# Kernel tuning notes

Hardware: AMD Instinct MI355X
Metric: run time of the kernel (lower is better)

The kernel has to match this reference:

```python
import jax, jax.numpy as jnp
import numpy as np

D_MODEL = 1024
NUM_HEADS = 16
D_K = D_MODEL // NUM_HEADS
THETA = 10000.0
BATCH = 4
SEQ = 2048


def _apply_rope(t, positions, theta):
    # t: (B, H, S, d_k); positions: (S,) int
    d_k = t.shape[-1]
    inv_freq = theta ** (-jnp.arange(0, d_k, 2, dtype=jnp.float32) / d_k)  # (d_k/2,)
    angles = positions.astype(jnp.float32)[:, None] * inv_freq[None, :]    # (S, d_k/2)
    cos = jnp.cos(angles)
    sin = jnp.sin(angles)
    x1 = t[..., 0::2]
    x2 = t[..., 1::2]
    r1 = x1 * cos - x2 * sin
    r2 = x1 * sin + x2 * cos
    # interleave back to (..., d_k)
    return jnp.stack([r1, r2], axis=-1).reshape(t.shape)


def setup_inputs() -> dict:
    key = jax.random.key(0)
    k0, k1, k2, k3, k4 = jax.random.split(key, 5)
    scale = 1.0 / np.sqrt(D_MODEL)
    return {
        "x": jax.random.normal(k0, (BATCH, SEQ, D_MODEL), dtype=jnp.float32),
        "wq": jax.random.normal(k1, (D_MODEL, D_MODEL), dtype=jnp.float32) * scale,
        "wk": jax.random.normal(k2, (D_MODEL, D_MODEL), dtype=jnp.float32) * scale,
        "wv": jax.random.normal(k3, (D_MODEL, D_MODEL), dtype=jnp.float32) * scale,
        "wo": jax.random.normal(k4, (D_MODEL, D_MODEL), dtype=jnp.float32) * scale,
        "token_positions": jnp.arange(SEQ, dtype=jnp.int32),
    }


def reference(x, wq, wk, wv, wo, token_positions):
    B, S, _ = x.shape
    H, dk = NUM_HEADS, D_K

    def proj(w):
        # Linear: y = x @ w.T, then split heads -> (B, H, S, d_k)
        y = jnp.einsum("bsd,ed->bse", x, w)
        return y.reshape(B, S, H, dk).transpose(0, 2, 1, 3)

    q = proj(wq)
    k = proj(wk)
    v = proj(wv)

    q = _apply_rope(q, token_positions, THETA)
    k = _apply_rope(k, token_positions, THETA)

    scores = jnp.einsum("bhqd,bhkd->bhqk", q, k) / jnp.sqrt(jnp.float32(dk))
    causal = jnp.tril(jnp.ones((S, S), dtype=bool))  # (S, S)
    scores = jnp.where(causal[None, None, :, :], scores, -jnp.inf)
    attn = jax.nn.softmax(scores, axis=-1)
    out = jnp.einsum("bhqk,bhkd->bhqd", attn, v)        # (B, H, S, d_k)
    out = out.transpose(0, 2, 1, 3).reshape(B, S, H * dk)
    return jnp.einsum("bse,de->bsd", out, wo)
```

## Files before the change

kernel.cpp:

```cpp
#include <hip/hip_runtime.h>
#include <hip/hip_bf16.h>

#define D_MODEL 1024
#define NHEADS 16
#define DKH 64
#define BATCH 4
#define SEQ 2048
#define BH_ (BATCH*NHEADS)
#define MROWS (BATCH*SEQ)

typedef __attribute__((ext_vector_type(8))) short bf16x8;
typedef __attribute__((ext_vector_type(4))) float f32x4;
typedef __attribute__((ext_vector_type(4))) short short4v;

static __device__ __forceinline__ unsigned short f2b(float f){
  union { float f; unsigned u; } v; v.f = f;
  unsigned u = v.u;
  return (unsigned short)((u + 0x7FFFu + ((u >> 16) & 1u)) >> 16);
}
static __device__ __forceinline__ float b2f(unsigned short h){
  union { unsigned u; float f; } v; v.u = ((unsigned)h) << 16; return v.f;
}

static __device__ __forceinline__ f32x4 mfma16(bf16x8 a, bf16x8 b, f32x4 c){
  return __builtin_amdgcn_mfma_f32_16x16x32_bf16(a, b, c, 0, 0, 0);
}

__global__ void cvt_bf16_kernel(const float* __restrict__ src,
                                unsigned short* __restrict__ dst, int n4){
  int i = blockIdx.x*blockDim.x + threadIdx.x;
  if (i >= n4) return;
  float4 f = ((const float4*)src)[i];
  short4v o;
  o.x = (short)f2b(f.x); o.y = (short)f2b(f.y);
  o.z = (short)f2b(f.z); o.w = (short)f2b(f.w);
  ((short4v*)dst)[i] = o;
}

#define BM 128
#define BN 128
#define BKG 64

template<int MODE>
__global__ __launch_bounds__(256) void gemm_nt(const unsigned short* __restrict__ A,
                                               const unsigned short* __restrict__ Bw,
                                               void* __restrict__ C,
                                               int M, int N, int K)
{
  __shared__ unsigned short As[BM*BKG];
  __shared__ unsigned short Bs[BN*BKG];
  const int t = threadIdx.x;
  const int lane = t & 63;
  const int wv = t >> 6;
  const int wr = wv >> 1, wc = wv & 1;
  const int l15 = lane & 15, l4 = lane >> 4;
  const int m0 = blockIdx.y*BM, n0 = blockIdx.x*BN;

  f32x4 acc[4][4] = {};

  int lrow[4], lsw[4], lke[4];
  #pragma unroll
  for (int i = 0; i < 4; ++i){
    int lin = t*64 + i*16;
    int row = lin >> 7;
    int koff = lin & 127;
    lrow[i] = row;
    lke[i]  = koff >> 1;
    lsw[i]  = row*128 + (koff ^ ((row & 7) << 4));
  }

  bf16x8 ra[4], rb[4];
  #pragma unroll
  for (int i = 0; i < 4; ++i){
    ra[i] = *(const bf16x8*)(A  + (size_t)(m0 + lrow[i])*K + lke[i]);
    rb[i] = *(const bf16x8*)(Bw + (size_t)(n0 + lrow[i])*K + lke[i]);
  }

  for (int kt = 0; kt < K; kt += BKG){
    if (kt) __syncthreads();
    #pragma unroll
    for (int i = 0; i < 4; ++i){
      *(bf16x8*)((char*)As + lsw[i]) = ra[i];
      *(bf16x8*)((char*)Bs + lsw[i]) = rb[i];
    }
    if (kt + BKG < K){
      #pragma unroll
      for (int i = 0; i < 4; ++i){
        ra[i] = *(const bf16x8*)(A  + (size_t)(m0 + lrow[i])*K + kt + BKG + lke[i]);
        rb[i] = *(const bf16x8*)(Bw + (size_t)(n0 + lrow[i])*K + kt + BKG + lke[i]);
      }
    }
    __syncthreads();
    #pragma unroll
    for (int kk = 0; kk < 2; ++kk){
      bf16x8 af[4], bfr[4];
      #pragma unroll
      for (int mi = 0; mi < 4; ++mi){
        int row = wr*64 + mi*16 + l15;
        int koff = kk*64 + l4*16;
        af[mi] = *(const bf16x8*)((const char*)As + row*128 + (koff ^ ((row & 7) << 4)));
      }
      #pragma unroll
      for (int ni = 0; ni < 4; ++ni){
        int row = wc*64 + ni*16 + l15;
        int koff = kk*64 + l4*16;
        bfr[ni] = *(const bf16x8*)((const char*)Bs + row*128 + (koff ^ ((row & 7) << 4)));
      }
      #pragma unroll
      for (int mi = 0; mi < 4; ++mi)
        #pragma unroll
        for (int ni = 0; ni < 4; ++ni)
          acc[mi][ni] = mfma16(af[mi], bfr[ni], acc[mi][ni]);
    }
  }

  #pragma unroll
  for (int mi = 0; mi < 4; ++mi)
    #pragma unroll
    for (int ni = 0; ni < 4; ++ni)
      #pragma unroll
      for (int r = 0; r < 4; ++r){
        int row = m0 + wr*64 + mi*16 + l4*4 + r;
        int col = n0 + wc*64 + ni*16 + l15;
        float v = acc[mi][ni][r];
        if (MODE == 0){
          int b = row >> 11, s = row & (SEQ-1);
          int h = col >> 6,  d = col & (DKH-1);
          ((unsigned short*)C)[((size_t)(b*NHEADS + h)*SEQ + s)*DKH + d] = f2b(v);
        } else {
          ((float*)C)[(size_t)row*N + col] = v;
        }
      }
}

__global__ void rope_kernel(unsigned int* __restrict__ qk,
                            const int* __restrict__ pos, int npairs){
  int i = blockIdx.x*blockDim.x + threadIdx.x;
  if (i >= npairs) return;
  int j = i & (DKH/2 - 1);
  int s = (i >> 5) & (SEQ-1);
  float p = (float)pos[s];
  float fr = expf(-((float)(2*j) * (1.0f/DKH)) * 9.210340371976184f);
  float ang = p * fr;
  float sn, cs;
  sincosf(ang, &sn, &cs);
  unsigned u = qk[i];
  float x1 = b2f((unsigned short)(u & 0xFFFFu));
  float x2 = b2f((unsigned short)(u >> 16));
  float r1 = x1*cs - x2*sn;
  float r2 = x1*sn + x2*cs;
  qk[i] = (unsigned)f2b(r1) | ((unsigned)f2b(r2) << 16);
}

__global__ void vtrans_kernel(const unsigned short* __restrict__ vin,
                              unsigned short* __restrict__ vt){
  __shared__ unsigned short tile[64][65];
  int bh = blockIdx.y;
  int s0 = blockIdx.x * 64;
  const unsigned short* src = vin + ((size_t)bh*SEQ + s0)*DKH;
  for (int i = threadIdx.x; i < 64*64; i += 256)
    tile[i >> 6][i & 63] = src[(size_t)(i >> 6)*DKH + (i & 63)];
  __syncthreads();
  unsigned short* dst = vt + (size_t)bh*DKH*SEQ + s0;
  for (int i = threadIdx.x; i < 64*64; i += 256)
    dst[(size_t)(i >> 6)*SEQ + (i & 63)] = tile[i & 63][i >> 6];
}

#define QW 32
#define QB 128
#define KVB 64

__global__ __launch_bounds__(256, 2) void attn_kernel(const unsigned short* __restrict__ Q,
                                                      const unsigned short* __restrict__ Kw,
                                                      const unsigned short* __restrict__ Vt,
                                                      unsigned short* __restrict__ Ob)
{
  __shared__ unsigned short Ks[2][KVB*64];
  __shared__ unsigned short Vs[2][KVB*64];
  __shared__ unsigned short Ps[4][QW*KVB];

  const int t = threadIdx.x;
  const int lane = t & 63;
  const int wv = t >> 6;
  const int l15 = lane & 15, l4 = lane >> 4;

  const int bid = blockIdx.x;
  const int bh = bid & (BH_-1);
  const int qt = (SEQ/QB - 1) - (bid >> 6);
  const int q0 = qt * QB;
  const int qw0 = q0 + wv*QW;

  const unsigned short* kg = Kw + (size_t)bh*SEQ*DKH;
  const unsigned short* vg = Vt + (size_t)bh*DKH*SEQ;
  const unsigned short* qg = Q  + ((size_t)bh*SEQ + qw0)*DKH;

  bf16x8 qa[2][2];
  #pragma unroll
  for (int qi = 0; qi < 2; ++qi)
    #pragma unroll
    for (int c = 0; c < 2; ++c)
      qa[qi][c] = *(const bf16x8*)(qg + (qi*16 + l15)*DKH + c*32 + l4*8);

  float m_r[2] = {-1e30f, -1e30f};
  float l_r[2] = {0.f, 0.f};
  f32x4 oacc[2][4] = {};

  const int srow = t >> 3;
  const int scb  = (t & 7) * 16;
  const int sko  = scb ^ ((srow & 7) << 4);
  const size_t vstride = (size_t)SEQ * 2;

  const int ntB   = q0/KVB + 2;
  const int twmax = (qw0 + QW - 1) >> 6;

  bf16x8 kl0, kl1, vl0, vl1;
  {
    const char* ksrc = (const char*)kg;
    const char* vsrc = (const char*)vg;
    kl0 = *(const bf16x8*)(ksrc + srow*128 + sko);
    kl1 = *(const bf16x8*)(ksrc + (srow+32)*128 + sko);
    vl0 = *(const bf16x8*)(vsrc + (size_t)srow*vstride + sko);
    vl1 = *(const bf16x8*)(vsrc + (size_t)(srow+32)*vstride + sko);
    *(bf16x8*)((char*)Ks[0] + srow*128 + scb)      = kl0;
    *(bf16x8*)((char*)Ks[0] + (srow+32)*128 + scb) = kl1;
    *(bf16x8*)((char*)Vs[0] + srow*128 + scb)      = vl0;
    *(bf16x8*)((char*)Vs[0] + (srow+32)*128 + scb) = vl1;
  }

  for (int tt = 0; tt < ntB; ++tt){
    const int cur = tt & 1;
    __syncthreads();
    const bool pre = (tt + 1 < ntB);
    if (pre){
      const size_t kvoff = (size_t)(tt+1) * KVB;
      const char* ksrc = (const char*)kg + kvoff*128;
      const char* vsrc = (const char*)vg + kvoff*2;
      kl0 = *(const bf16x8*)(ksrc + srow*128 + sko);
      kl1 = *(const bf16x8*)(ksrc + (srow+32)*128 + sko);
      vl0 = *(const bf16x8*)(vsrc + (size_t)srow*vstride + sko);
      vl1 = *(const bf16x8*)(vsrc + (size_t)(srow+32)*vstride + sko);
    }

    if (tt <= twmax){
      const char* kb = (const char*)Ks[cur];
      const char* vb = (const char*)Vs[cur];
      char* pb = (char*)Ps[wv];
      const int sw = (l15 & 7) << 4;

      f32x4 sacc[4][2];
      #pragma unroll
      for (int kt = 0; kt < 4; ++kt){
        const int krow = kt*16 + l15;
        bf16x8 kf0 = *(const bf16x8*)(kb + krow*128 + ((l4*16) ^ sw));
        bf16x8 kf1 = *(const bf16x8*)(kb + krow*128 + ((64 + l4*16) ^ sw));
        #pragma unroll
        for (int qi = 0; qi < 2; ++qi){
          f32x4 a = {};
          a = mfma16(kf0, qa[qi][0], a);
          a = mfma16(kf1, qa[qi][1], a);
          sacc[kt][qi] = a;
        }
      }

      const int kv0 = tt * KVB;
      #pragma unroll
      for (int qi = 0; qi < 2; ++qi){
        const int qrow = qw0 + qi*16 + l15;
        float p[16];
        float mloc = -1e30f;
        #pragma unroll
        for (int kt = 0; kt < 4; ++kt)
          #pragma unroll
          for (int r = 0; r < 4; ++r){
            int kvg = kv0 + kt*16 + l4*4 + r;
            float x = sacc[kt][qi][r] * 0.125f;
            x = (kvg > qrow) ? -1e30f : x;
            p[kt*4+r] = x;
            mloc = fmaxf(mloc, x);
          }
        mloc = fmaxf(mloc, __shfl_xor(mloc, 16));
        mloc = fmaxf(mloc, __shfl_xor(mloc, 32));
        float mn = fmaxf(m_r[qi], mloc);
        float alpha = __expf(m_r[qi] - mn);
        m_r[qi] = mn;
        float rs = 0.f;
        #pragma unroll
        for (int i = 0; i < 16; ++i){ p[i] = __expf(p[i] - mn); rs += p[i]; }
        rs += __shfl_xor(rs, 16);
        rs += __shfl_xor(rs, 32);
        l_r[qi] = l_r[qi]*alpha + rs;
        float ar[4];
        #pragma unroll
        for (int r = 0; r < 4; ++r) ar[r] = __shfl(alpha, l4*4 + r);
        #pragma unroll
        for (int dt = 0; dt < 4; ++dt)
          #pragma unroll
          for (int r = 0; r < 4; ++r) oacc[qi][dt][r] *= ar[r];
        char* pr = pb + (qi*16 + l15)*128;
        #pragma unroll
        for (int kt = 0; kt < 4; ++kt){
          unsigned u0, u1;
          asm("v_cvt_pk_bf16_f32 %0, %1, %2" : "=v"(u0) : "v"(p[kt*4+0]), "v"(p[kt*4+1]));
          asm("v_cvt_pk_bf16_f32 %0, %1, %2" : "=v"(u1) : "v"(p[kt*4+2]), "v"(p[kt*4+3]));
          unsigned long long uu = (unsigned long long)u0 | ((unsigned long long)u1 << 32);
          *(unsigned long long*)(pr + ((kt*32 + l4*8) ^ sw)) = uu;
        }
      }

      bf16x8 pa[2][2];
      #pragma unroll
      for (int qi = 0; qi < 2; ++qi){
        const char* pr = pb + (qi*16 + l15)*128;
        pa[qi][0] = *(const bf16x8*)(pr + ((l4*16) ^ sw));
        pa[qi][1] = *(const bf16x8*)(pr + ((64 + l4*16) ^ sw));
      }

      #pragma unroll
      for (int dt = 0; dt < 4; ++dt){
        const int vrow = dt*16 + l15;
        bf16x8 vf0 = *(const bf16x8*)(vb + vrow*128 + ((l4*16) ^ sw));
        bf16x8 vf1 = *(const bf16x8*)(vb + vrow*128 + ((64 + l4*16) ^ sw));
        #pragma unroll
        for (int qi = 0; qi < 2; ++qi){
          oacc[qi][dt] = mfma16(pa[qi][0], vf0, oacc[qi][dt]);
          oacc[qi][dt] = mfma16(pa[qi][1], vf1, oacc[qi][dt]);
        }
      }
    }

    if (pre){
      char* kd = (char*)Ks[cur^1];
      char* vd = (char*)Vs[cur^1];
      *(bf16x8*)(kd + srow*128 + scb)      = kl0;
      *(bf16x8*)(kd + (srow+32)*128 + scb) = kl1;
      *(bf16x8*)(vd + srow*128 + scb)      = vl0;
      *(bf16x8*)(vd + (srow+32)*128 + scb) = vl1;
    }
  }

  const int b = bh >> 4, h = bh & 15;
  #pragma unroll
  for (int qi = 0; qi < 2; ++qi){
    float inv = 1.0f / l_r[qi];
    float ir[4];
    #pragma unroll
    for (int r = 0; r < 4; ++r) ir[r] = __shfl(inv, l4*4 + r);
    #pragma unroll
    for (int r = 0; r < 4; ++r){
      int q = qw0 + qi*16 + l4*4 + r;
      unsigned short* orow = Ob + ((size_t)(b*SEQ + q))*D_MODEL + h*DKH;
      #pragma unroll
      for (int dt = 0; dt < 4; ++dt)
        orow[dt*16 + l15] = f2b(oacc[qi][dt][r] * inv * 0.f + oacc[qi][dt][r] * ir[r]);
    }
  }
}

extern "C" void kernel_launch(void* const* d_in, const int* in_sizes, int n_in,
                              void* d_out, int out_size, void* d_ws, size_t ws_size,
                              hipStream_t stream)
{
  const float* x  = (const float*)d_in[0];
  const float* wq = (const float*)d_in[1];
  const float* wk = (const float*)d_in[2];
  const float* wv = (const float*)d_in[3];
  const float* wo = (const float*)d_in[4];
  const int* tp   = (const int*)d_in[5];
  float* out = (float*)d_out;

  unsigned short* ws = (unsigned short*)d_ws;
  size_t off = 0;
  unsigned short* xb  = ws + off; off += (size_t)MROWS*D_MODEL;
  unsigned short* wqb = ws + off; off += (size_t)D_MODEL*D_MODEL;
  unsigned short* wkb = ws + off; off += (size_t)D_MODEL*D_MODEL;
  unsigned short* wvb = ws + off; off += (size_t)D_MODEL*D_MODEL;
  unsigned short* wob = ws + off; off += (size_t)D_MODEL*D_MODEL;
  unsigned short* qw  = ws + off; off += (size_t)BH_*SEQ*DKH;
  unsigned short* kw  = ws + off; off += (size_t)BH_*SEQ*DKH;
  unsigned short* vtmp= ws + off; off += (size_t)BH_*SEQ*DKH;
  unsigned short* vt  = ws + off; off += (size_t)BH_*SEQ*DKH;
  unsigned short* ao  = vtmp;

  const int NW = D_MODEL*D_MODEL/4;
  cvt_bf16_kernel<<<(MROWS*D_MODEL/4 + 255)/256, 256, 0, stream>>>(x,  xb,  MROWS*D_MODEL/4);
  cvt_bf16_kernel<<<(NW + 255)/256, 256, 0, stream>>>(wq, wqb, NW);
  cvt_bf16_kernel<<<(NW + 255)/256, 256, 0, stream>>>(wk, wkb, NW);
  cvt_bf16_kernel<<<(NW + 255)/256, 256, 0, stream>>>(wv, wvb, NW);
  cvt_bf16_kernel<<<(NW + 255)/256, 256, 0, stream>>>(wo, wob, NW);

  dim3 gg(D_MODEL/BN, MROWS/BM);
  gemm_nt<0><<<gg, 256, 0, stream>>>(xb, wqb, qw,   MROWS, D_MODEL, D_MODEL);
  gemm_nt<0><<<gg, 256, 0, stream>>>(xb, wkb, kw,   MROWS, D_MODEL, D_MODEL);
  gemm_nt<0><<<gg, 256, 0, stream>>>(xb, wvb, vtmp, MROWS, D_MODEL, D_MODEL);

  const int npairs = BH_*SEQ*(DKH/2);
  rope_kernel<<<(npairs + 255)/256, 256, 0, stream>>>((unsigned int*)qw, tp, npairs);
  rope_kernel<<<(npairs + 255)/256, 256, 0, stream>>>((unsigned int*)kw, tp, npairs);

  vtrans_kernel<<<dim3(SEQ/64, BH_), 256, 0, stream>>>(vtmp, vt);

  attn_kernel<<<BH_*(SEQ/QB), 256, 0, stream>>>(qw, kw, vt, ao);

  gemm_nt<1><<<gg, 256, 0, stream>>>(ao, wob, out, MROWS, D_MODEL, D_MODEL);
}
```

Measured before the change: 301.8 us.

## Fuse QKV GEMM, use direct-to-LDS loads, and streamline attention softmax

```diff
diff --git a/kernel.cpp b/kernel.cpp
--- a/kernel.cpp
+++ b/kernel.cpp
@@ -24,6 +24,20 @@
 
 static __device__ __forceinline__ f32x4 mfma16(bf16x8 a, bf16x8 b, f32x4 c){
   return __builtin_amdgcn_mfma_f32_16x16x32_bf16(a, b, c, 0, 0, 0);
+}
+
+static __device__ __forceinline__ float fexp2(float x){
+#if __has_builtin(__builtin_amdgcn_exp2f)
+  return __builtin_amdgcn_exp2f(x);
+#else
+  float r; asm("v_exp_f32 %0, %1" : "=v"(r) : "v"(x)); return r;
+#endif
+}
+
+static __device__ __forceinline__ void gload_lds16(const unsigned short* g, void* l){
+  __builtin_amdgcn_global_load_lds((const __attribute__((address_space(1))) void*)g,
+                                   (__attribute__((address_space(3))) void*)l,
+                                   16, 0, 0);
 }
 
 __global__ void cvt_bf16_kernel(const float* __restrict__ src,
@@ -37,15 +51,30 @@
   ((short4v*)dst)[i] = o;
 }
 
+__global__ void cvt_w_kernel(const float* __restrict__ wq, const float* __restrict__ wk,
+                             const float* __restrict__ wv, const float* __restrict__ wo,
+                             unsigned short* __restrict__ wcat, unsigned short* __restrict__ wob){
+  int i = blockIdx.x*blockDim.x + threadIdx.x;
+  int seg = i >> 18;
+  int j = i & 0x3FFFF;
+  const float* s = (seg==0) ? wq : (seg==1) ? wk : (seg==2) ? wv : wo;
+  unsigned short* d = (seg < 3) ? (wcat + ((size_t)seg << 20)) : wob;
+  float4 f = ((const float4*)s)[j];
+  short4v o;
+  o.x = (short)f2b(f.x); o.y = (short)f2b(f.y);
+  o.z = (short)f2b(f.z); o.w = (short)f2b(f.w);
+  ((short4v*)d)[j] = o;
+}
+
 #define BM 128
 #define BN 128
 #define BKG 64
 
 template<int MODE>
-__global__ __launch_bounds__(256) void gemm_nt(const unsigned short* __restrict__ A,
-                                               const unsigned short* __restrict__ Bw,
-                                               void* __restrict__ C,
-                                               int M, int N, int K)
+__global__ __launch_bounds__(256, 3) void gemm_nt(const unsigned short* __restrict__ A,
+                                                  const unsigned short* __restrict__ Bw,
+                                                  void* __restrict__ C,
+                                                  int M, int N, int K)
 {
   __shared__ unsigned short As[BM*BKG];
   __shared__ unsigned short Bs[BN*BKG];
@@ -58,54 +87,28 @@
 
   f32x4 acc[4][4] = {};
 
-  int lrow[4], lsw[4], lke[4];
-  #pragma unroll
-  for (int i = 0; i < 4; ++i){
-    int lin = t*64 + i*16;
-    int row = lin >> 7;
-    int koff = lin & 127;
-    lrow[i] = row;
-    lke[i]  = koff >> 1;
-    lsw[i]  = row*128 + (koff ^ ((row & 7) << 4));
-  }
-
-  bf16x8 ra[4], rb[4];
-  #pragma unroll
-  for (int i = 0; i < 4; ++i){
-    ra[i] = *(const bf16x8*)(A  + (size_t)(m0 + lrow[i])*K + lke[i]);
-    rb[i] = *(const bf16x8*)(Bw + (size_t)(n0 + lrow[i])*K + lke[i]);
-  }
+  const int srow = lane >> 3;
+  const int sce  = (lane & 7) * 8;
 
   for (int kt = 0; kt < K; kt += BKG){
-    if (kt) __syncthreads();
-    #pragma unroll
-    for (int i = 0; i < 4; ++i){
-      *(bf16x8*)((char*)As + lsw[i]) = ra[i];
-      *(bf16x8*)((char*)Bs + lsw[i]) = rb[i];
-    }
-    if (kt + BKG < K){
-      #pragma unroll
-      for (int i = 0; i < 4; ++i){
-        ra[i] = *(const bf16x8*)(A  + (size_t)(m0 + lrow[i])*K + kt + BKG + lke[i]);
-        rb[i] = *(const bf16x8*)(Bw + (size_t)(n0 + lrow[i])*K + kt + BKG + lke[i]);
-      }
+    __syncthreads();
+    #pragma unroll
+    for (int jj = 0; jj < 4; ++jj){
+      const int i = wv + jj*4;
+      const int row = i*8 + srow;
+      gload_lds16(A  + (size_t)(m0 + row)*K + kt + sce, (char*)As + i*1024 + lane*16);
+      gload_lds16(Bw + (size_t)(n0 + row)*K + kt + sce, (char*)Bs + i*1024 + lane*16);
     }
     __syncthreads();
     #pragma unroll
     for (int kk = 0; kk < 2; ++kk){
       bf16x8 af[4], bfr[4];
       #pragma unroll
-      for (int mi = 0; mi < 4; ++mi){
-        int row = wr*64 + mi*16 + l15;
-        int koff = kk*64 + l4*16;
-        af[mi] = *(const bf16x8*)((const char*)As + row*128 + (koff ^ ((row & 7) << 4)));
-      }
-      #pragma unroll
-      for (int ni = 0; ni < 4; ++ni){
-        int row = wc*64 + ni*16 + l15;
-        int koff = kk*64 + l4*16;
-        bfr[ni] = *(const bf16x8*)((const char*)Bs + row*128 + (koff ^ ((row & 7) << 4)));
-      }
+      for (int mi = 0; mi < 4; ++mi)
+        af[mi] = *(const bf16x8*)((const char*)As + (wr*64 + mi*16 + l15)*128 + kk*64 + l4*16);
+      #pragma unroll
+      for (int ni = 0; ni < 4; ++ni)
+        bfr[ni] = *(const bf16x8*)((const char*)Bs + (wc*64 + ni*16 + l15)*128 + kk*64 + l4*16);
       #pragma unroll
       for (int mi = 0; mi < 4; ++mi)
         #pragma unroll
@@ -124,9 +127,12 @@
         int col = n0 + wc*64 + ni*16 + l15;
         float v = acc[mi][ni][r];
         if (MODE == 0){
+          int which = col >> 10;
+          int cl = col & 1023;
           int b = row >> 11, s = row & (SEQ-1);
-          int h = col >> 6,  d = col & (DKH-1);
-          ((unsigned short*)C)[((size_t)(b*NHEADS + h)*SEQ + s)*DKH + d] = f2b(v);
+          int h = cl >> 6,  d = cl & (DKH-1);
+          ((unsigned short*)C)[(size_t)which*((size_t)BH_*SEQ*DKH)
+                               + ((size_t)(b*NHEADS + h)*SEQ + s)*DKH + d] = f2b(v);
         } else {
           ((float*)C)[(size_t)row*N + col] = v;
         }
@@ -201,6 +207,7 @@
     for (int c = 0; c < 2; ++c)
       qa[qi][c] = *(const bf16x8*)(qg + (qi*16 + l15)*DKH + c*32 + l4*8);
 
+  const float KAPPA = 0.125f * 1.4426950408889634f;
   float m_r[2] = {-1e30f, -1e30f};
   float l_r[2] = {0.f, 0.f};
   f32x4 oacc[2][4] = {};
@@ -246,6 +253,7 @@
       const char* vb = (const char*)Vs[cur];
       char* pb = (char*)Ps[wv];
       const int sw = (l15 & 7) << 4;
+      const bool needmask = (tt == twmax);
 
       f32x4 sacc[4][2];
       #pragma unroll
@@ -272,30 +280,39 @@
         for (int kt = 0; kt < 4; ++kt)
           #pragma unroll
           for (int r = 0; r < 4; ++r){
-            int kvg = kv0 + kt*16 + l4*4 + r;
-            float x = sacc[kt][qi][r] * 0.125f;
-            x = (kvg > qrow) ? -1e30f : x;
+            float x = sacc[kt][qi][r] * KAPPA;
+            if (needmask){
+              int kvg = kv0 + kt*16 + l4*4 + r;
+              x = (kvg > qrow) ? -1e30f : x;
+            }
             p[kt*4+r] = x;
             mloc = fmaxf(mloc, x);
           }
         mloc = fmaxf(mloc, __shfl_xor(mloc, 16));
         mloc = fmaxf(mloc, __shfl_xor(mloc, 32));
-        float mn = fmaxf(m_r[qi], mloc);
-        float alpha = __expf(m_r[qi] - mn);
-        m_r[qi] = mn;
+
+        const bool skip = __all(mloc - m_r[qi] <= 12.0f);
+        float mn = m_r[qi];
+        if (!skip){
+          mn = fmaxf(m_r[qi], mloc);
+          float alpha = fexp2(m_r[qi] - mn);
+          m_r[qi] = mn;
+          l_r[qi] *= alpha;
+          float ar[4];
+          #pragma unroll
+          for (int r = 0; r < 4; ++r) ar[r] = __shfl(alpha, l4*4 + r);
+          #pragma unroll
+          for (int dt = 0; dt < 4; ++dt)
+            #pragma unroll
+            for (int r = 0; r < 4; ++r) oacc[qi][dt][r] *= ar[r];
+        }
         float rs = 0.f;
         #pragma unroll
-        for (int i = 0; i < 16; ++i){ p[i] = __expf(p[i] - mn); rs += p[i]; }
+        for (int i = 0; i < 16; ++i){ p[i] = fexp2(p[i] - mn); rs += p[i]; }
         rs += __shfl_xor(rs, 16);
         rs += __shfl_xor(rs, 32);
-        l_r[qi] = l_r[qi]*alpha + rs;
-        float ar[4];
-        #pragma unroll
-        for (int r = 0; r < 4; ++r) ar[r] = __shfl(alpha, l4*4 + r);
-        #pragma unroll
-        for (int dt = 0; dt < 4; ++dt)
-          #pragma unroll
-          for (int r = 0; r < 4; ++r) oacc[qi][dt][r] *= ar[r];
+        l_r[qi] += rs;
+
         char* pr = pb + (qi*16 + l15)*128;
         #pragma unroll
         for (int kt = 0; kt < 4; ++kt){
@@ -351,7 +368,7 @@
       unsigned short* orow = Ob + ((size_t)(b*SEQ + q))*D_MODEL + h*DKH;
       #pragma unroll
       for (int dt = 0; dt < 4; ++dt)
-        orow[dt*16 + l15] = f2b(oacc[qi][dt][r] * inv * 0.f + oacc[qi][dt][r] * ir[r]);
+        orow[dt*16 + l15] = f2b(oacc[qi][dt][r] * ir[r]);
     }
   }
 }
@@ -370,28 +387,19 @@
 
   unsigned short* ws = (unsigned short*)d_ws;
   size_t off = 0;
-  unsigned short* xb  = ws + off; off += (size_t)MROWS*D_MODEL;
-  unsigned short* wqb = ws + off; off += (size_t)D_MODEL*D_MODEL;
-  unsigned short* wkb = ws + off; off += (size_t)D_MODEL*D_MODEL;
-  unsigned short* wvb = ws + off; off += (size_t)D_MODEL*D_MODEL;
-  unsigned short* wob = ws + off; off += (size_t)D_MODEL*D_MODEL;
-  unsigned short* qw  = ws + off; off += (size_t)BH_*SEQ*DKH;
-  unsigned short* kw  = ws + off; off += (size_t)BH_*SEQ*DKH;
-  unsigned short* vtmp= ws + off; off += (size_t)BH_*SEQ*DKH;
-  unsigned short* vt  = ws + off; off += (size_t)BH_*SEQ*DKH;
-  unsigned short* ao  = vtmp;
-
-  const int NW = D_MODEL*D_MODEL/4;
-  cvt_bf16_kernel<<<(MROWS*D_MODEL/4 + 255)/256, 256, 0, stream>>>(x,  xb,  MROWS*D_MODEL/4);
-  cvt_bf16_kernel<<<(NW + 255)/256, 256, 0, stream>>>(wq, wqb, NW);
-  cvt_bf16_kernel<<<(NW + 255)/256, 256, 0, stream>>>(wk, wkb, NW);
-  cvt_bf16_kernel<<<(NW + 255)/256, 256, 0, stream>>>(wv, wvb, NW);
-  cvt_bf16_kernel<<<(NW + 255)/256, 256, 0, stream>>>(wo, wob, NW);
-
-  dim3 gg(D_MODEL/BN, MROWS/BM);
-  gemm_nt<0><<<gg, 256, 0, stream>>>(xb, wqb, qw,   MROWS, D_MODEL, D_MODEL);
-  gemm_nt<0><<<gg, 256, 0, stream>>>(xb, wkb, kw,   MROWS, D_MODEL, D_MODEL);
-  gemm_nt<0><<<gg, 256, 0, stream>>>(xb, wvb, vtmp, MROWS, D_MODEL, D_MODEL);
+  unsigned short* xb   = ws + off; off += (size_t)MROWS*D_MODEL;
+  unsigned short* wcat = ws + off; off += (size_t)3*D_MODEL*D_MODEL;
+  unsigned short* wob  = ws + off; off += (size_t)D_MODEL*D_MODEL;
+  unsigned short* qw   = ws + off; off += (size_t)BH_*SEQ*DKH;
+  unsigned short* kw   = ws + off; off += (size_t)BH_*SEQ*DKH;
+  unsigned short* vtmp = ws + off; off += (size_t)BH_*SEQ*DKH;
+  unsigned short* vt   = ws + off; off += (size_t)BH_*SEQ*DKH;
+  unsigned short* ao   = vtmp;
+
+  cvt_bf16_kernel<<<(MROWS*D_MODEL/4 + 255)/256, 256, 0, stream>>>(x, xb, MROWS*D_MODEL/4);
+  cvt_w_kernel<<<(4*262144 + 255)/256, 256, 0, stream>>>(wq, wk, wv, wo, wcat, wob);
+
+  gemm_nt<0><<<dim3(3*D_MODEL/BN, MROWS/BM), 256, 0, stream>>>(xb, wcat, qw, MROWS, 3*D_MODEL, D_MODEL);
 
   const int npairs = BH_*SEQ*(DKH/2);
   rope_kernel<<<(npairs + 255)/256, 256, 0, stream>>>((unsigned int*)qw, tp, npairs);
@@ -401,5 +409,5 @@
 
   attn_kernel<<<BH_*(SEQ/QB), 256, 0, stream>>>(qw, kw, vt, ao);
 
-  gemm_nt<1><<<gg, 256, 0, stream>>>(ao, wob, out, MROWS, D_MODEL, D_MODEL);
-}
+  gemm_nt<1><<<dim3(D_MODEL/BN, MROWS/BM), 256, 0, stream>>>(ao, wob, out, MROWS, D_MODEL, D_MODEL);
+}
```

After: 282.9 us. -6.3%, faster.
